# Kernel tuning notes

Hardware: AMD Instinct MI355X
Metric: run time of the kernel (lower is better)

## Reference

```python
import jax, jax.numpy as jnp
import numpy as np

CLAMP = 5.0

def setup_inputs() -> dict:
    key = jax.random.key(0)
    k1, k2, k3, k4, k5 = jax.random.split(key, 5)
    B, S, D, R = 4, 4096, 2048, 16
    v = jax.random.normal(k1, (B, S, D), dtype=jnp.float32)
    x = jax.random.normal(k2, (B, S, D), dtype=jnp.float32)
    # params; match torch init scale (0.001) for U/W; V is zero-init in the module,
    # but use small random so the modulation branch is exercised.
    U = jax.random.normal(k3, (D, R), dtype=jnp.float32) * 0.001
    W = jax.random.normal(k4, (D, R), dtype=jnp.float32) * 0.001
    Vw = jax.random.normal(k5, (1, D), dtype=jnp.float32) * 0.01
    return {"v": v, "x": x, "U": U, "W": W, "Vw": Vw}

def reference(v, x, U, W, Vw):
    # proj: [B,S,R] ; sq elementwise ; out: [B,S,D]
    proj = jnp.einsum('bsd,dr->bsr', v, U)
    sq = proj * proj
    out = jnp.einsum('bsr,dr->bsd', sq, W)
    # dynamic curvature modulation: sigmoid(V^T x), V is Linear(dim,1,no bias)
    modulation = jax.nn.sigmoid(jnp.einsum('bsd,od->bso', x, Vw))  # [B,S,1]
    out = out * (1.0 + modulation)
    return jnp.clip(out, -CLAMP, CLAMP)
```

## Files before the change

kernel.cpp:

```cpp
#include <hip/hip_runtime.h>
#include <math.h>


typedef short bf16x8 __attribute__((ext_vector_type(8)));
typedef float f32x4  __attribute__((ext_vector_type(4)));

constexpr int D_DIM   = 2048;
constexpr int R_DIM   = 16;
constexpr int MROWS   = 16;
constexpr int THREADS = 256;
constexpr int KSLICE  = 512;
constexpr int KSTEPS  = KSLICE / 32;

__device__ __forceinline__ unsigned f2bf(float f) {
    unsigned u = __float_as_uint(f);
    return (u + 0x7fffu + ((u >> 16) & 1u)) >> 16;
}
__device__ __forceinline__ float bf2f(unsigned b) { return __uint_as_float(b << 16); }
__device__ __forceinline__ float clamp5(float v) { return fminf(fmaxf(v, -5.0f), 5.0f); }
__device__ __forceinline__ float dot4f(float4 a, float4 b) {
    return a.x * b.x + a.y * b.y + a.z * b.z + a.w * b.w;
}

extern "C" __global__ void __launch_bounds__(THREADS, 4)
lrc_mfma(const float* __restrict__ v, const float* __restrict__ x,
         const float* __restrict__ U, const float* __restrict__ W,
         const float* __restrict__ Vw, float* __restrict__ out, int nrows)
{
    __shared__ float proj_lds[4][MROWS][R_DIM];
    __shared__ float xv_lds[4][MROWS];
    __shared__ float sq_lds[MROWS][R_DIM];
    __shared__ float fac_lds[MROWS];

    const int tid  = threadIdx.x;
    const int lane = tid & 63;
    const int wave = tid >> 6;
    const int l16  = lane & 15;
    const int lk   = lane >> 4;
    const int row0 = blockIdx.x * MROWS;

    int grow = row0 + l16;
    if (grow >= nrows) grow = nrows - 1;
    const float* vp = v + (size_t)grow * D_DIM;
    const float* xp = x + (size_t)grow * D_DIM;

    f32x4 acc = {0.f, 0.f, 0.f, 0.f};
    float xv = 0.f;
    const int kbase = wave * KSLICE + lk * 8;

    #pragma unroll 4
    for (int s = 0; s < KSTEPS; ++s) {
        const int k = kbase + s * 32;
        const float4 va = *reinterpret_cast<const float4*>(vp + k);
        const float4 vb = *reinterpret_cast<const float4*>(vp + k + 4);
        const float4 xa = *reinterpret_cast<const float4*>(xp + k);
        const float4 xb = *reinterpret_cast<const float4*>(xp + k + 4);
        const float4 wa = *reinterpret_cast<const float4*>(Vw + k);
        const float4 wb = *reinterpret_cast<const float4*>(Vw + k + 4);

        const float* up = U + (size_t)k * R_DIM + l16;
        bf16x8 bu;
        #pragma unroll
        for (int e = 0; e < 8; ++e) bu[e] = (short)f2bf(up[e * R_DIM]);

        const float vf[8] = {va.x, va.y, va.z, va.w, vb.x, vb.y, vb.z, vb.w};
        bf16x8 ah, al;
        #pragma unroll
        for (int e = 0; e < 8; ++e) {
            const unsigned h = f2bf(vf[e]);
            ah[e] = (short)h;
            al[e] = (short)f2bf(vf[e] - bf2f(h));
        }
        acc = __builtin_amdgcn_mfma_f32_16x16x32_bf16(ah, bu, acc, 0, 0, 0);
        acc = __builtin_amdgcn_mfma_f32_16x16x32_bf16(al, bu, acc, 0, 0, 0);

        xv += dot4f(xa, wa) + dot4f(xb, wb);
    }
    xv += __shfl_xor(xv, 16, 64);
    xv += __shfl_xor(xv, 32, 64);

    #pragma unroll
    for (int i = 0; i < 4; ++i) proj_lds[wave][lk * 4 + i][l16] = acc[i];
    if (lk == 0) xv_lds[wave][l16] = xv;
    __syncthreads();

    {
        const int m = tid >> 4, r = tid & 15;
        const float p = proj_lds[0][m][r] + proj_lds[1][m][r]
                      + proj_lds[2][m][r] + proj_lds[3][m][r];
        sq_lds[m][r] = p * p;
        if (tid < MROWS) {
            const float s = xv_lds[0][tid] + xv_lds[1][tid]
                          + xv_lds[2][tid] + xv_lds[3][tid];
            fac_lds[tid] = 1.0f + 1.0f / (1.0f + __expf(-s));
        }
    }
    __syncthreads();

    bf16x8 asq;
    #pragma unroll
    for (int e = 0; e < 8; ++e) {
        const int kk = lk * 8 + e;
        asq[e] = (kk < R_DIM) ? (short)f2bf(sq_lds[l16][kk]) : (short)0;
    }
    float fr[4];
    #pragma unroll
    for (int i = 0; i < 4; ++i) fr[i] = fac_lds[lk * 4 + i];

    #pragma unroll 4
    for (int c = 0; c < 32; ++c) {
        const int d0 = wave * 512 + c * 16;
        bf16x8 bw;
        if (lk < 2) {
            const float* wp = W + (size_t)(d0 + l16) * R_DIM + lk * 8;
            const float4 q0 = *reinterpret_cast<const float4*>(wp);
            const float4 q1 = *reinterpret_cast<const float4*>(wp + 4);
            bw[0] = (short)f2bf(q0.x); bw[1] = (short)f2bf(q0.y);
            bw[2] = (short)f2bf(q0.z); bw[3] = (short)f2bf(q0.w);
            bw[4] = (short)f2bf(q1.x); bw[5] = (short)f2bf(q1.y);
            bw[6] = (short)f2bf(q1.z); bw[7] = (short)f2bf(q1.w);
        } else {
            #pragma unroll
            for (int e = 0; e < 8; ++e) bw[e] = 0;
        }
        f32x4 o = {0.f, 0.f, 0.f, 0.f};
        o = __builtin_amdgcn_mfma_f32_16x16x32_bf16(asq, bw, o, 0, 0, 0);
        #pragma unroll
        for (int i = 0; i < 4; ++i) {
            const int rr = row0 + lk * 4 + i;
            if (rr < nrows)
                out[(size_t)rr * D_DIM + d0 + l16] = clamp5(o[i] * fr[i]);
        }
    }
}

extern "C" void kernel_launch(void* const* d_in, const int* in_sizes, int n_in,
                              void* d_out, int out_size, void* d_ws, size_t ws_size,
                              hipStream_t stream) {
    const float* v  = (const float*)d_in[0];
    const float* x  = (const float*)d_in[1];
    const float* U  = (const float*)d_in[2];
    const float* W  = (const float*)d_in[3];
    const float* Vw = (const float*)d_in[4];
    float* out = (float*)d_out;

    const int nrows = in_sizes[0] / D_DIM;
    const int grid  = (nrows + MROWS - 1) / MROWS;

    lrc_mfma<<<grid, THREADS, 0, stream>>>(v, x, U, W, Vw, out, nrows);
}
```

Before: 105.4 us.

## Stage U as transposed bf16 in LDS and use 8 waves per block

Each block now first converts U to bf16 and writes it transposed into a padded LDS buffer of about 66 KB. The projection MFMA then reads its B operand with one vector LDS load instead of eight strided global loads plus conversions. The block grows to 512 threads (8 waves), each covering half the K slice and half the output columns. The cost is that every block reloads and converts all of U into LDS, and the large LDS footprint limits how many blocks fit per CU.

```diff
diff --git a/kernel.cpp b/kernel.cpp
--- a/kernel.cpp
+++ b/kernel.cpp
@@ -8,9 +8,11 @@
 constexpr int D_DIM   = 2048;
 constexpr int R_DIM   = 16;
 constexpr int MROWS   = 16;
-constexpr int THREADS = 256;
-constexpr int KSLICE  = 512;
+constexpr int THREADS = 512;
+constexpr int WAVES   = 8;
+constexpr int KSLICE  = 256;
 constexpr int KSTEPS  = KSLICE / 32;
+constexpr int DP      = 2072;
 
 __device__ __forceinline__ unsigned f2bf(float f) {
     unsigned u = __float_as_uint(f);
@@ -22,14 +24,15 @@
     return a.x * b.x + a.y * b.y + a.z * b.z + a.w * b.w;
 }
 
-extern "C" __global__ void __launch_bounds__(THREADS, 4)
+extern "C" __global__ void __launch_bounds__(THREADS)
 lrc_mfma(const float* __restrict__ v, const float* __restrict__ x,
          const float* __restrict__ U, const float* __restrict__ W,
          const float* __restrict__ Vw, float* __restrict__ out, int nrows)
 {
-    __shared__ float proj_lds[4][MROWS][R_DIM];
-    __shared__ float xv_lds[4][MROWS];
-    __shared__ float sq_lds[MROWS][R_DIM];
+    __shared__ unsigned short u_lds[R_DIM * DP];
+    __shared__ float proj_lds[WAVES][MROWS][17];
+    __shared__ float xv_lds[WAVES][MROWS];
+    __shared__ float sq_lds[MROWS][17];
     __shared__ float fac_lds[MROWS];
 
     const int tid  = threadIdx.x;
@@ -39,97 +42,121 @@
     const int lk   = lane >> 4;
     const int row0 = blockIdx.x * MROWS;
 
-    int grow = row0 + l16;
-    if (grow >= nrows) grow = nrows - 1;
-    const float* vp = v + (size_t)grow * D_DIM;
-    const float* xp = x + (size_t)grow * D_DIM;
-
-    f32x4 acc = {0.f, 0.f, 0.f, 0.f};
-    float xv = 0.f;
-    const int kbase = wave * KSLICE + lk * 8;
-
-    #pragma unroll 4
-    for (int s = 0; s < KSTEPS; ++s) {
-        const int k = kbase + s * 32;
-        const float4 va = *reinterpret_cast<const float4*>(vp + k);
-        const float4 vb = *reinterpret_cast<const float4*>(vp + k + 4);
-        const float4 xa = *reinterpret_cast<const float4*>(xp + k);
-        const float4 xb = *reinterpret_cast<const float4*>(xp + k + 4);
-        const float4 wa = *reinterpret_cast<const float4*>(Vw + k);
-        const float4 wb = *reinterpret_cast<const float4*>(Vw + k + 4);
-
-        const float* up = U + (size_t)k * R_DIM + l16;
-        bf16x8 bu;
+    {
+        const float* up = U + (size_t)tid * 4 * R_DIM;
+        float c0[R_DIM], c1[R_DIM], c2[R_DIM], c3[R_DIM];
         #pragma unroll
-        for (int e = 0; e < 8; ++e) bu[e] = (short)f2bf(up[e * R_DIM]);
-
-        const float vf[8] = {va.x, va.y, va.z, va.w, vb.x, vb.y, vb.z, vb.w};
-        bf16x8 ah, al;
+        for (int q = 0; q < 4; ++q) {
+            *reinterpret_cast<float4*>(&c0[q * 4]) = reinterpret_cast<const float4*>(up)[q];
+            *reinterpret_cast<float4*>(&c1[q * 4]) = reinterpret_cast<const float4*>(up + 16)[q];
+            *reinterpret_cast<float4*>(&c2[q * 4]) = reinterpret_cast<const float4*>(up + 32)[q];
+            *reinterpret_cast<float4*>(&c3[q * 4]) = reinterpret_cast<const float4*>(up + 48)[q];
+        }
         #pragma unroll
-        for (int e = 0; e < 8; ++e) {
-            const unsigned h = f2bf(vf[e]);
-            ah[e] = (short)h;
-            al[e] = (short)f2bf(vf[e] - bf2f(h));
-        }
-        acc = __builtin_amdgcn_mfma_f32_16x16x32_bf16(ah, bu, acc, 0, 0, 0);
-        acc = __builtin_amdgcn_mfma_f32_16x16x32_bf16(al, bu, acc, 0, 0, 0);
-
-        xv += dot4f(xa, wa) + dot4f(xb, wb);
-    }
-    xv += __shfl_xor(xv, 16, 64);
-    xv += __shfl_xor(xv, 32, 64);
-
-    #pragma unroll
-    for (int i = 0; i < 4; ++i) proj_lds[wave][lk * 4 + i][l16] = acc[i];
-    if (lk == 0) xv_lds[wave][l16] = xv;
-    __syncthreads();
-
-    {
-        const int m = tid >> 4, r = tid & 15;
-        const float p = proj_lds[0][m][r] + proj_lds[1][m][r]
-                      + proj_lds[2][m][r] + proj_lds[3][m][r];
-        sq_lds[m][r] = p * p;
-        if (tid < MROWS) {
-            const float s = xv_lds[0][tid] + xv_lds[1][tid]
-                          + xv_lds[2][tid] + xv_lds[3][tid];
-            fac_lds[tid] = 1.0f + 1.0f / (1.0f + __expf(-s));
+        for (int r = 0; r < R_DIM; ++r) {
+            uint2 pk;
+            pk.x = f2bf(c0[r]) | (f2bf(c1[r]) << 16);
+            pk.y = f2bf(c2[r]) | (f2bf(c3[r]) << 16);
+            *reinterpret_cast<uint2*>(&u_lds[r * DP + tid * 4]) = pk;
         }
     }
     __syncthreads();
 
-    bf16x8 asq;
-    #pragma unroll
-    for (int e = 0; e < 8; ++e) {
-        const int kk = lk * 8 + e;
-        asq[e] = (kk < R_DIM) ? (short)f2bf(sq_lds[l16][kk]) : (short)0;
+    {
+        int grow = row0 + l16;
+        if (grow >= nrows) grow = nrows - 1;
+        const float* vp = v + (size_t)grow * D_DIM;
+        const float* xp = x + (size_t)grow * D_DIM;
+
+        f32x4 acc = {0.f, 0.f, 0.f, 0.f};
+        float xv = 0.f;
+        const int kb = wave * KSLICE + lk * 8;
+
+        #pragma unroll
+        for (int s = 0; s < KSTEPS; ++s) {
+            const int k = kb + s * 32;
+            const float4 va = *reinterpret_cast<const float4*>(vp + k);
+            const float4 vb = *reinterpret_cast<const float4*>(vp + k + 4);
+            const float4 xa = *reinterpret_cast<const float4*>(xp + k);
+            const float4 xb = *reinterpret_cast<const float4*>(xp + k + 4);
+            const float4 wa = *reinterpret_cast<const float4*>(Vw + k);
+            const float4 wb = *reinterpret_cast<const float4*>(Vw + k + 4);
+
+            const bf16x8 bu = *reinterpret_cast<const bf16x8*>(&u_lds[l16 * DP + k]);
+
+            const float vf[8] = {va.x, va.y, va.z, va.w, vb.x, vb.y, vb.z, vb.w};
+            bf16x8 ah, al;
+            #pragma unroll
+            for (int e = 0; e < 8; ++e) {
+                const unsigned h = f2bf(vf[e]);
+                ah[e] = (short)h;
+                al[e] = (short)f2bf(vf[e] - bf2f(h));
+            }
+            acc = __builtin_amdgcn_mfma_f32_16x16x32_bf16(ah, bu, acc, 0, 0, 0);
+            acc = __builtin_amdgcn_mfma_f32_16x16x32_bf16(al, bu, acc, 0, 0, 0);
+
+            xv += dot4f(xa, wa) + dot4f(xb, wb);
+        }
+        xv += __shfl_xor(xv, 16, 64);
+        xv += __shfl_xor(xv, 32, 64);
+
+        #pragma unroll
+        for (int i = 0; i < 4; ++i) proj_lds[wave][lk * 4 + i][l16] = acc[i];
+        if (lk == 0) xv_lds[wave][l16] = xv;
     }
-    float fr[4];
-    #pragma unroll
-    for (int i = 0; i < 4; ++i) fr[i] = fac_lds[lk * 4 + i];
+    __syncthreads();
 
-    #pragma unroll 4
-    for (int c = 0; c < 32; ++c) {
-        const int d0 = wave * 512 + c * 16;
-        bf16x8 bw;
-        if (lk < 2) {
-            const float* wp = W + (size_t)(d0 + l16) * R_DIM + lk * 8;
-            const float4 q0 = *reinterpret_cast<const float4*>(wp);
-            const float4 q1 = *reinterpret_cast<const float4*>(wp + 4);
-            bw[0] = (short)f2bf(q0.x); bw[1] = (short)f2bf(q0.y);
-            bw[2] = (short)f2bf(q0.z); bw[3] = (short)f2bf(q0.w);
-            bw[4] = (short)f2bf(q1.x); bw[5] = (short)f2bf(q1.y);
-            bw[6] = (short)f2bf(q1.z); bw[7] = (short)f2bf(q1.w);
-        } else {
+    if (tid < MROWS * R_DIM) {
+        const int m = tid >> 4, r = tid & 15;
+        float p = 0.f;
+        #pragma unroll
+        for (int w = 0; w < WAVES; ++w) p += proj_lds[w][m][r];
+        sq_lds[m][r] = p * p;
+    }
+    if (tid < MROWS) {
+        float s = 0.f;
+        #pragma unroll
+        for (int w = 0; w < WAVES; ++w) s += xv_lds[w][tid];
+        fac_lds[tid] = 1.0f + 1.0f / (1.0f + __expf(-s));
+    }
+    __syncthreads();
+
+    {
+        bf16x8 asq;
+        #pragma unroll
+        for (int e = 0; e < 8; ++e) {
+            const int kk = lk * 8 + e;
+            asq[e] = (kk < R_DIM) ? (short)f2bf(sq_lds[l16][kk]) : (short)0;
+        }
+        float fr[4];
+        #pragma unroll
+        for (int i = 0; i < 4; ++i) fr[i] = fac_lds[lk * 4 + i];
+
+        const int dbase = wave * 256;
+        #pragma unroll 4
+        for (int c = 0; c < 16; ++c) {
+            const int d0 = dbase + c * 16;
+            bf16x8 bw;
+            if (lk < 2) {
+                const float* wp = W + (size_t)(d0 + l16) * R_DIM + lk * 8;
+                const float4 q0 = *reinterpret_cast<const float4*>(wp);
+                const float4 q1 = *reinterpret_cast<const float4*>(wp + 4);
+                bw[0] = (short)f2bf(q0.x); bw[1] = (short)f2bf(q0.y);
+                bw[2] = (short)f2bf(q0.z); bw[3] = (short)f2bf(q0.w);
+                bw[4] = (short)f2bf(q1.x); bw[5] = (short)f2bf(q1.y);
+                bw[6] = (short)f2bf(q1.z); bw[7] = (short)f2bf(q1.w);
+            } else {
+                #pragma unroll
+                for (int e = 0; e < 8; ++e) bw[e] = 0;
+            }
+            f32x4 o = {0.f, 0.f, 0.f, 0.f};
+            o = __builtin_amdgcn_mfma_f32_16x16x32_bf16(asq, bw, o, 0, 0, 0);
             #pragma unroll
-            for (int e = 0; e < 8; ++e) bw[e] = 0;
-        }
-        f32x4 o = {0.f, 0.f, 0.f, 0.f};
-        o = __builtin_amdgcn_mfma_f32_16x16x32_bf16(asq, bw, o, 0, 0, 0);
-        #pragma unroll
-        for (int i = 0; i < 4; ++i) {
-            const int rr = row0 + lk * 4 + i;
-            if (rr < nrows)
-                out[(size_t)rr * D_DIM + d0 + l16] = clamp5(o[i] * fr[i]);
+            for (int i = 0; i < 4; ++i) {
+                const int rr = row0 + lk * 4 + i;
+                if (rr < nrows)
+                    out[(size_t)rr * D_DIM + d0 + l16] = clamp5(o[i] * fr[i]);
+            }
         }
     }
 }
```

Result: slower. 109.9 us (+4.2%).
